# Performance work log

Measured on AMD Instinct MI355X. Metric: run time of the kernel, lower is better.

## Reference

```python
import jax, jax.numpy as jnp
import numpy as np
from jax.scipy.special import erf

B, T, D, H = 256, 128, 128, 1024  # batch, seq_len, enc_in, hid_dim
SIGMA = 0.5  # stochastic-gate sigma (STG FeatureSelector)


def _uniform(key, shape, std):
    return jax.random.uniform(key, shape, jnp.float32, -std, std)


def setup_inputs() -> dict:
    key = jax.random.key(0)
    ks = jax.random.split(key, 16)
    std = 1.0 / np.sqrt(H)
    inp = {
        "x": jax.random.normal(ks[0], (B, T, D), jnp.float32),
        # s_lstm
        "s_x2h_w": _uniform(ks[1], (4 * H, D), std),
        "s_x2h_b": _uniform(ks[2], (4 * H,), std),
        "s_h2h_w": _uniform(ks[3], (4 * H, H), std),
        "s_h2h_b": _uniform(ks[4], (4 * H,), std),
        # p_lstm
        "p_x2h_w": _uniform(ks[5], (4 * H, D), std),
        "p_x2h_b": _uniform(ks[6], (4 * H,), std),
        "p_h2h_w": _uniform(ks[7], (4 * H, H), std),
        "p_h2h_b": _uniform(ks[8], (4 * H,), std),
        # p_fc: hid -> 2*enc_in
        "p_fc_w": _uniform(ks[9], (2 * D, H), std),
        "p_fc_b": _uniform(ks[10], (2 * D,), std),
        # FeatureSelector mu layer: hid -> enc_in
        "fs_w": _uniform(ks[11], (D, H), std),
        "fs_b": _uniform(ks[12], (D,), std),
    }
    return inp


def _lstm_cell(x, h, c, wx, bx, wh, bh):
    gates = x @ wx.T + bx + h @ wh.T + bh          # [B, 4H]
    i, f, g, o = jnp.split(gates, 4, axis=1)
    cy = c * jax.nn.sigmoid(f) + jax.nn.sigmoid(i) * jnp.tanh(g)
    hy = jax.nn.sigmoid(o) * jnp.tanh(cy)
    return hy, cy


def _forward(x, s_x2h_w, s_x2h_b, s_h2h_w, s_h2h_b,
             p_x2h_w, p_x2h_b, p_h2h_w, p_h2h_b,
             p_fc_w, p_fc_b, fs_w, fs_b):
    b = x.shape[0]
    xt = jnp.swapaxes(x, 0, 1)  # [T, B, D] time-major
    sqrt2 = jnp.sqrt(jnp.float32(2.0))

    def step(carry, xs):
        hn, cn, hn2, cn2, mask_prev, xhat0_prev = carry
        x_t, x_tp1 = xs
        # at seq==0 mask_prev=1, xhat0_prev=0 -> input is exactly x_t
        inp = mask_prev * x_t + (1.0 - mask_prev) * xhat0_prev
        hn, cn = _lstm_cell(inp, hn, cn, s_x2h_w, s_x2h_b, s_h2h_w, s_h2h_b)
        # FeatureSelector (eval: noise = 0)
        mu = hn @ fs_w.T + fs_b                     # [B, D]
        z = mu
        mask = jnp.clip(z + 0.5, 0.0, 1.0)          # hard sigmoid gate
        reg = 0.5 * (1.0 + erf((mu + 0.5) / (SIGMA * sqrt2)))  # Phi((mu+0.5)/sigma)
        hn2, cn2 = _lstm_cell(mask * x_tp1, hn2, cn2, p_x2h_w, p_x2h_b, p_h2h_w, p_h2h_b)
        xhat = (hn2 @ p_fc_w.T + p_fc_b).reshape(b, 2, D)
        xhat0, xhat1 = xhat[:, 0, :], xhat[:, 1, :]
        mu_det = jax.lax.stop_gradient(mu)          # torch.tensor(numpy) detaches
        prob_det = jax.lax.stop_gradient(reg)
        outs = (mask, xhat0, xhat1, reg, mu_det, prob_det, z)
        return (hn, cn, hn2, cn2, mask, xhat0), outs

    h0 = jnp.zeros((b, H), x.dtype)
    carry0 = (h0, h0, h0, h0, jnp.ones((b, D), x.dtype), jnp.zeros((b, D), x.dtype))
    _, outs = jax.lax.scan(step, carry0, (xt[:-1], xt[1:]))
    # each out: [T-1, B, D] -> [B, T-1, D]
    return tuple(jnp.swapaxes(o, 0, 1) for o in outs)


def reference(x, s_x2h_w, s_x2h_b, s_h2h_w, s_h2h_b,
              p_x2h_w, p_x2h_b, p_h2h_w, p_h2h_b,
              p_fc_w, p_fc_b, fs_w, fs_b):
    return _forward(x, s_x2h_w, s_x2h_b, s_h2h_w, s_h2h_b,
                    p_x2h_w, p_x2h_b, p_h2h_w, p_h2h_b,
                    p_fc_w, p_fc_b, fs_w, fs_b)
```

## Files before the change

### kernel.cpp

```cpp
#include <hip/hip_runtime.h>
#include <math.h>

#define BB 256
#define TT 128
#define DD 128
#define HH 1024
#define G4 4096
#define TOUT 127
#define OSZ (BB * TOUT * DD)
#define NKB 36
#define ACTE (16 * NKB * 512)

typedef __bf16 bf16x8 __attribute__((ext_vector_type(8)));
typedef float f32x4 __attribute__((ext_vector_type(4)));
typedef unsigned short u16;
typedef unsigned int u32;
typedef unsigned long long u64;

#define MFMA16 __builtin_amdgcn_mfma_f32_16x16x32_bf16

__device__ inline u16 f2bf(float f) {
    union { float f; u32 u; } v; v.f = f;
    u32 r = v.u + 0x7FFFu + ((v.u >> 16) & 1u);
    return (u16)(r >> 16);
}
__device__ inline float fsig(float x)  { return __fdividef(1.0f, 1.0f + __expf(-x)); }
__device__ inline float ftanh(float x) { return __fdividef(2.0f, 1.0f + __expf(-2.0f * x)) - 1.0f; }

__device__ __forceinline__ bf16x8 ld_act(const u16* p) {
    union { u64 q[2]; bf16x8 v; } u;
    u.q[0] = __hip_atomic_load((u64*)p,     __ATOMIC_RELAXED, __HIP_MEMORY_SCOPE_AGENT);
    u.q[1] = __hip_atomic_load((u64*)p + 1, __ATOMIC_RELAXED, __HIP_MEMORY_SCOPE_AGENT);
    return u.v;
}
__device__ __forceinline__ void st_u32(u16* p, u32 v) {
    __hip_atomic_store((u32*)p, v, __ATOMIC_RELAXED, __HIP_MEMORY_SCOPE_AGENT);
}

__device__ __forceinline__ void gbar(u32* bars, u32 gen) {
    asm volatile("s_waitcnt vmcnt(0)" ::: "memory");
    __syncthreads();
    if (threadIdx.x == 0)
        __hip_atomic_fetch_add(&bars[(blockIdx.x & 31) << 4], 1u,
                               __ATOMIC_RELAXED, __HIP_MEMORY_SCOPE_AGENT);
    if (threadIdx.x < 32) {
        while (__hip_atomic_load(&bars[threadIdx.x << 4],
                                 __ATOMIC_RELAXED, __HIP_MEMORY_SCOPE_AGENT) < gen * 8u)
            __builtin_amdgcn_s_sleep(4);
    }
    __syncthreads();
}

struct SArgs {
    u16 *acts, *actp;
    const u16 *wS, *wP, *fswb, *pfcb;
    const float *bS, *bP, *fsb, *pfb, *x;
    float* mbuf;
    float* out;
    u32* bars;
};

__device__ __forceinline__ void lstm_phase(
    const u16* __restrict__ act, const u16* __restrict__ wb,
    const float* __restrict__ bias, float* __restrict__ cst ,
    u16* __restrict__ hact, float* __restrict__ red ,
    u64* __restrict__ a_lds ,
    int bid, int w, int lane)
{
    const int tid = threadIdx.x;
    const int bm = bid >> 5, bn = bid & 31;
    const int kg = w >> 2, wv = w & 3;

    {
        const u64* src = (const u64*)(act + (size_t)bm * 2 * NKB * 512);
#pragma unroll
        for (int u = 0; u < 18; ++u) {
            int idx = tid + u * 512;
            a_lds[idx] = __hip_atomic_load(&src[idx], __ATOMIC_RELAXED,
                                           __HIP_MEMORY_SCOPE_AGENT);
        }
    }
    __syncthreads();

    const u16* ab = (const u16*)a_lds;
    const u16* a0p = ab + (((0 * NKB) + kg * 18) * 64 + lane) * 8;
    const u16* a1p = ab + (((1 * NKB) + kg * 18) * 64 + lane) * 8;
    const u16* b0p = wb + (((size_t)(bn * 8 + wv * 2 + 0) * NKB + kg * 18) * 64 + lane) * 8;
    const u16* b1p = wb + (((size_t)(bn * 8 + wv * 2 + 1) * NKB + kg * 18) * 64 + lane) * 8;

    f32x4 acc[2][2] = {};
    bf16x8 bc0 = *(const bf16x8*)(b0p);
    bf16x8 bc1 = *(const bf16x8*)(b1p);
#pragma unroll 6
    for (int it = 0; it < 18; ++it) {
        bf16x8 bn0, bn1;
        if (it < 17) {
            bn0 = *(const bf16x8*)(b0p + (it + 1) * 512);
            bn1 = *(const bf16x8*)(b1p + (it + 1) * 512);
        }
        bf16x8 a0 = *(const bf16x8*)(a0p + it * 512);
        bf16x8 a1 = *(const bf16x8*)(a1p + it * 512);
        acc[0][0] = MFMA16(a0, bc0, acc[0][0], 0, 0, 0);
        acc[0][1] = MFMA16(a0, bc1, acc[0][1], 0, 0, 0);
        acc[1][0] = MFMA16(a1, bc0, acc[1][0], 0, 0, 0);
        acc[1][1] = MFMA16(a1, bc1, acc[1][1], 0, 0, 0);
        if (it < 17) { bc0 = bn0; bc1 = bn1; }
    }

    if (kg == 1) {
#pragma unroll
        for (int mi = 0; mi < 2; ++mi)
#pragma unroll
        for (int bi = 0; bi < 2; ++bi)
            *(f32x4*)&red[(((((wv << 1) | mi) << 1) | bi) << 8) + (lane << 2)] = acc[mi][bi];
    }
    __syncthreads();

    if (kg == 0) {
        const int col = lane & 15, row4 = (lane >> 4) << 2, g0 = lane & 3;
#pragma unroll
        for (int mi = 0; mi < 2; ++mi)
#pragma unroll
        for (int bi = 0; bi < 2; ++bi) {
            f32x4 s1 = *(const f32x4*)&red[(((((wv << 1) | mi) << 1) | bi) << 8) + (lane << 2)];
            const int n = bn * 128 + (wv * 2 + bi) * 16 + col;
            const float bv = bias[n];
#pragma unroll
            for (int rr = 0; rr < 4; ++rr) {
                float v = acc[mi][bi][rr] + s1[rr] + bv;
                float v1 = __shfl_xor(v, 1);
                float v2 = __shfl_xor(v, 2);
                float v3 = __shfl_xor(v, 3);
                const int m = bm * 32 + mi * 16 + row4 + rr;
                const int j = n >> 2;
                u32 hbits = 0;
                if (g0 == 0) {
                    const int ml = mi * 16 + row4 + rr;
                    const int jl = j - bn * 32;
                    float cp = cst[ml * 32 + jl];
                    float cy = cp * fsig(v1) + fsig(v) * ftanh(v2);
                    float hy = fsig(v3) * ftanh(cy);
                    cst[ml * 32 + jl] = cy;
                    hbits = (u32)f2bf(hy);
                }
                u32 pv = hbits | (((u32)__shfl_xor((int)hbits, 4)) << 16);
                if ((lane & 7) == 0)
                    st_u32(&hact[(((size_t)(m >> 4) * NKB + (4 + (j >> 5))) * 64 +
                                  ((m & 15) + (((j >> 3) & 3) << 4))) * 8 + (j & 7)], pv);
            }
        }
    }
}

__global__ __launch_bounds__(512, 2) void k_scan(SArgs A)
{
    __shared__ __align__(16) u64 a_lds[9216];
    __shared__ __align__(16) float red[4096];
    __shared__ float cst[2][32][32];

    const int bid = blockIdx.x, tid = threadIdx.x;
    const int w = tid >> 6, lane = tid & 63;

    for (int i = tid; i < 2 * 32 * 32; i += 512) ((float*)cst)[i] = 0.f;

    float* o_mask = A.out;
    float* o_x0   = A.out + 1 * (size_t)OSZ;
    float* o_x1   = A.out + 2 * (size_t)OSZ;
    float* o_reg  = A.out + 3 * (size_t)OSZ;
    float* o_mu   = A.out + 4 * (size_t)OSZ;
    float* o_prob = A.out + 5 * (size_t)OSZ;
    float* o_z    = A.out + 6 * (size_t)OSZ;

    u32 gen = 0;

    for (int t = 0; t < TOUT; ++t) {
        const u16* s_cur = A.acts + (size_t)(t & 1) * ACTE;
        u16*       s_nxt = A.acts + (size_t)((t + 1) & 1) * ACTE;
        u16*       p_cur = A.actp + (size_t)(t & 1) * ACTE;
        u16*       p_nxt = A.actp + (size_t)((t + 1) & 1) * ACTE;

        lstm_phase(s_cur, A.wS, A.bS, &cst[0][0][0], s_nxt, red, a_lds, bid, w, lane);
        gbar(A.bars, ++gen);

        if (bid < 128) {
            const int bm = bid >> 3, bn = bid & 7;
            f32x4 acc = {};
#pragma unroll
            for (int i = 0; i < 4; ++i) {
                const int kb = (w << 2) + i;
                bf16x8 av = ld_act(s_nxt + (((size_t)bm * NKB + 4 + kb) * 64 + lane) * 8);
                bf16x8 bv = *(const bf16x8*)(A.fswb + (((size_t)bn * 32 + kb) * 64 + lane) * 8);
                acc = MFMA16(av, bv, acc, 0, 0, 0);
            }
            *(f32x4*)&red[(w * 64 + lane) << 2] = acc;
            __syncthreads();
            if (tid < 256) {
                const int m16 = tid >> 4, d16 = tid & 15;
                const int rl = ((m16 >> 2) << 4) | d16, rr = m16 & 3;
                float v = 0.f;
#pragma unroll
                for (int ww = 0; ww < 8; ++ww) v += red[((ww * 64 + rl) << 2) + rr];
                const int m = (bm << 4) + m16, d = (bn << 4) + d16;
                float mu = v + A.fsb[d];
                float mask = fminf(fmaxf(mu + 0.5f, 0.f), 1.f);
                float reg = 0.5f * (1.0f + erff((mu + 0.5f) * 1.41421356237f));
                const size_t o = (size_t)m * (TOUT * DD) + (size_t)t * DD + d;
                o_mask[o] = mask; o_reg[o] = reg; o_mu[o] = mu; o_prob[o] = reg; o_z[o] = mu;
                __hip_atomic_store(&A.mbuf[m * DD + d], mask,
                                   __ATOMIC_RELAXED, __HIP_MEMORY_SCOPE_AGENT);
                float xv = A.x[(size_t)m * (TT * DD) + (size_t)(t + 1) * DD + d];
                u32 xb = (u32)f2bf(mask * xv);
                u32 pv = xb | (((u32)__shfl_xor((int)xb, 1)) << 16);
                if ((d16 & 1) == 0)
                    st_u32(&p_cur[(((size_t)(m >> 4) * NKB + (d >> 5)) * 64 +
                                   ((m & 15) + (((d >> 3) & 3) << 4))) * 8 + (d & 7)], pv);
            }
        }
        gbar(A.bars, ++gen);

        lstm_phase(p_cur, A.wP, A.bP, &cst[1][0][0], p_nxt, red, a_lds, bid, w, lane);
        gbar(A.bars, ++gen);

        {
            const int bm = bid >> 4, bn = bid & 15;
            f32x4 acc = {};
#pragma unroll
            for (int i = 0; i < 4; ++i) {
                const int kb = (w << 2) + i;
                bf16x8 av = ld_act(p_nxt + (((size_t)bm * NKB + 4 + kb) * 64 + lane) * 8);
                bf16x8 bv = *(const bf16x8*)(A.pfcb + (((size_t)bn * 32 + kb) * 64 + lane) * 8);
                acc = MFMA16(av, bv, acc, 0, 0, 0);
            }
            *(f32x4*)&red[(w * 64 + lane) << 2] = acc;
            __syncthreads();
            if (tid < 256) {
                const int m16 = tid >> 4, d16 = tid & 15;
                const int rl = ((m16 >> 2) << 4) | d16, rr = m16 & 3;
                float v = 0.f;
#pragma unroll
                for (int ww = 0; ww < 8; ++ww) v += red[((ww * 64 + rl) << 2) + rr];
                const int m = (bm << 4) + m16, n = (bn << 4) + d16;
                v += A.pfb[n];
                const size_t ob = (size_t)m * (TOUT * DD) + (size_t)t * DD;
                if (bn < 8) {
                    o_x0[ob + n] = v;
                    float mk = __hip_atomic_load(&A.mbuf[m * DD + n],
                                                 __ATOMIC_RELAXED, __HIP_MEMORY_SCOPE_AGENT);
                    float xv = A.x[(size_t)m * (TT * DD) + (size_t)(t + 1) * DD + n];
                    u32 ib = (u32)f2bf(mk * xv + (1.f - mk) * v);
                    u32 pv = ib | (((u32)__shfl_xor((int)ib, 1)) << 16);
                    if ((d16 & 1) == 0)
                        st_u32(&s_nxt[(((size_t)(m >> 4) * NKB + (n >> 5)) * 64 +
                                       ((m & 15) + (((n >> 3) & 3) << 4))) * 8 + (n & 7)], pv);
                } else {
                    o_x1[ob + (n - DD)] = v;
                }
            }
        }
        gbar(A.bars, ++gen);
    }
}


__global__ void k_wgates(const float* __restrict__ wx, const float* __restrict__ wh,
                         u16* __restrict__ blob) {
    int i = blockIdx.x * 256 + threadIdx.x;
    if (i >= 256 * NKB * 64) return;
    int lane = i & 63, cblk = (i >> 6) % NKB, rblk = (i >> 6) / NKB;
    int n = (rblk << 4) | (lane & 15);
    int c = (cblk << 5) + ((lane >> 4) << 3);
    int orow = ((n & 3) << 10) | (n >> 2);
    const float* s = (cblk < 4) ? (wx + (size_t)orow * DD + c)
                                : (wh + (size_t)orow * HH + (c - 128));
    u16* d = blob + (size_t)i * 8;
#pragma unroll
    for (int k = 0; k < 8; ++k) d[k] = f2bf(s[k]);
}

__global__ void k_wplain(const float* __restrict__ wsrc, u16* __restrict__ blob,
                         int nblk, int K) {
    int CB = K >> 5;
    int i = blockIdx.x * 256 + threadIdx.x;
    if (i >= nblk * CB * 64) return;
    int lane = i & 63, cblk = (i >> 6) % CB, rblk = (i >> 6) / CB;
    int r = (rblk << 4) | (lane & 15);
    int c = (cblk << 5) + ((lane >> 4) << 3);
    const float* s = wsrc + (size_t)r * K + c;
    u16* d = blob + (size_t)i * 8;
#pragma unroll
    for (int k = 0; k < 8; ++k) d[k] = f2bf(s[k]);
}

__global__ void k_bias2(const float* __restrict__ bx, const float* __restrict__ bh,
                        float* __restrict__ dst) {
    int r = blockIdx.x * 256 + threadIdx.x;
    if (r < G4) {
        int o = ((r & 3) << 10) | (r >> 2);
        dst[r] = bx[o] + bh[o];
    }
}

__global__ void k_zero(u16* acts, u16* actp, u32* bars) {
    size_t i = (size_t)blockIdx.x * 256 + threadIdx.x;
    if (i < 2 * (size_t)ACTE) { acts[i] = 0; actp[i] = 0; }
    if (i < 512) bars[i] = 0;
}

__global__ void k_fillx(const float* __restrict__ x, u16* __restrict__ acts) {
    int i = blockIdx.x * 256 + threadIdx.x;
    if (i >= BB * DD) return;
    int m = i >> 7, d = i & 127;
    acts[(((size_t)(m >> 4) * NKB + (d >> 5)) * 64 +
          ((m & 15) + (((d >> 3) & 3) << 4))) * 8 + (d & 7)] =
        f2bf(x[(size_t)m * (TT * DD) + d]);
}

extern "C" void kernel_launch(void* const* d_in, const int* in_sizes, int n_in,
                              void* d_out, int out_size, void* d_ws, size_t ws_size,
                              hipStream_t stream) {
    const float* x       = (const float*)d_in[0];
    const float* s_x2h_w = (const float*)d_in[1];
    const float* s_x2h_b = (const float*)d_in[2];
    const float* s_h2h_w = (const float*)d_in[3];
    const float* s_h2h_b = (const float*)d_in[4];
    const float* p_x2h_w = (const float*)d_in[5];
    const float* p_x2h_b = (const float*)d_in[6];
    const float* p_h2h_w = (const float*)d_in[7];
    const float* p_h2h_b = (const float*)d_in[8];
    const float* p_fc_w  = (const float*)d_in[9];
    const float* p_fc_b  = (const float*)d_in[10];
    const float* fs_w    = (const float*)d_in[11];
    const float* fs_b    = (const float*)d_in[12];

    char* ws = (char*)d_ws;
    size_t off = 0;
    auto alloc = [&](size_t bytes) { void* p = ws + off; off += (bytes + 255) & ~(size_t)255; return p; };
    u16*   wS   = (u16*)  alloc((size_t)G4 * 1152 * 2);
    u16*   wP   = (u16*)  alloc((size_t)G4 * 1152 * 2);
    u16*   fswb = (u16*)  alloc((size_t)8 * 32 * 512 * 2);
    u16*   pfcb = (u16*)  alloc((size_t)16 * 32 * 512 * 2);
    float* bS   = (float*)alloc((size_t)G4 * 4);
    float* bP   = (float*)alloc((size_t)G4 * 4);
    u16*   acts = (u16*)  alloc((size_t)2 * ACTE * 2);
    u16*   actp = (u16*)  alloc((size_t)2 * ACTE * 2);
    float* mbuf = (float*)alloc((size_t)BB * DD * 4);
    u32*   bars = (u32*)  alloc(2048);

    k_wgates<<<dim3(2304), 256, 0, stream>>>(s_x2h_w, s_h2h_w, wS);
    k_wgates<<<dim3(2304), 256, 0, stream>>>(p_x2h_w, p_h2h_w, wP);
    k_wplain<<<dim3(64),  256, 0, stream>>>(fs_w, fswb, 8, 1024);
    k_wplain<<<dim3(128), 256, 0, stream>>>(p_fc_w, pfcb, 16, 1024);
    k_bias2<<<dim3(16), 256, 0, stream>>>(s_x2h_b, s_h2h_b, bS);
    k_bias2<<<dim3(16), 256, 0, stream>>>(p_x2h_b, p_h2h_b, bP);
    k_zero<<<dim3(2304), 256, 0, stream>>>(acts, actp, bars);
    k_fillx<<<dim3(128), 256, 0, stream>>>(x, acts);

    SArgs sa;
    sa.acts = acts; sa.actp = actp;
    sa.wS = wS; sa.wP = wP; sa.fswb = fswb; sa.pfcb = pfcb;
    sa.bS = bS; sa.bP = bP; sa.fsb = fs_b; sa.pfb = p_fc_b; sa.x = x;
    sa.mbuf = mbuf; sa.out = (float*)d_out; sa.bars = bars;

    void* kargs[] = { &sa };
    hipError_t e = hipLaunchCooperativeKernel((const void*)k_scan, dim3(256), dim3(512),
                                              kargs, 0, stream);
    if (e != hipSuccess) {
        k_scan<<<dim3(256), dim3(512), 0, stream>>>(sa);
    }
}
```

Baseline: 5.063 ms.

## Overlap FS/FC heads with next LSTM h2h GEMM using flag-based sync

Restructures the persistent scan so the recurrent h2h part of each LSTM gate GEMM (K=1024, from an LDS copy prefetched during the previous phase) overlaps with the feature-selector and p_fc GEMMs, done by a subset of waves. Point-to-point per-tile flags replace two of the four grid barriers per step, and the x-input slice (K=128) is added afterward in a tail. The grid barrier is centralized: block 0 polls the counters and publishes an epoch. The K-split reduction through shared memory is removed, with each wave doing the full K for one column tile. This cuts barrier count and serialization per timestep, at the cost of more complex synchronization and one block per CU.

```diff
diff --git a/kernel.cpp b/kernel.cpp
--- a/kernel.cpp
+++ b/kernel.cpp
@@ -27,237 +27,290 @@
 __device__ inline float fsig(float x)  { return __fdividef(1.0f, 1.0f + __expf(-x)); }
 __device__ inline float ftanh(float x) { return __fdividef(2.0f, 1.0f + __expf(-2.0f * x)) - 1.0f; }
 
-__device__ __forceinline__ bf16x8 ld_act(const u16* p) {
+__device__ __forceinline__ u64 ldc64(const u64* p) {
+    return __hip_atomic_load(p, __ATOMIC_RELAXED, __HIP_MEMORY_SCOPE_AGENT);
+}
+__device__ __forceinline__ bf16x8 ldc128(const u16* p) {
     union { u64 q[2]; bf16x8 v; } u;
-    u.q[0] = __hip_atomic_load((u64*)p,     __ATOMIC_RELAXED, __HIP_MEMORY_SCOPE_AGENT);
-    u.q[1] = __hip_atomic_load((u64*)p + 1, __ATOMIC_RELAXED, __HIP_MEMORY_SCOPE_AGENT);
+    u.q[0] = ldc64((const u64*)p);
+    u.q[1] = ldc64((const u64*)p + 1);
     return u.v;
 }
-__device__ __forceinline__ void st_u32(u16* p, u32 v) {
+__device__ __forceinline__ void stc32(u16* p, u32 v) {
     __hip_atomic_store((u32*)p, v, __ATOMIC_RELAXED, __HIP_MEMORY_SCOPE_AGENT);
 }
-
-__device__ __forceinline__ void gbar(u32* bars, u32 gen) {
+__device__ __forceinline__ void stcf(float* p, float v) {
+    __hip_atomic_store(p, v, __ATOMIC_RELAXED, __HIP_MEMORY_SCOPE_AGENT);
+}
+__device__ __forceinline__ float ldcf(const float* p) {
+    return __hip_atomic_load(p, __ATOMIC_RELAXED, __HIP_MEMORY_SCOPE_AGENT);
+}
+
+struct SArgs {
+    u16 *acts, *actp;
+    const u16 *wS, *wP, *fswb, *pfcb;
+    const float *bS, *bP, *fsb, *pfb, *x;
+    float *mbuf, *out;
+    u32 *bars, *epoch, *flags;
+};
+
+__device__ __forceinline__ void gbar(u32* bars, u32* epoch, u32 gen) {
     asm volatile("s_waitcnt vmcnt(0)" ::: "memory");
     __syncthreads();
     if (threadIdx.x == 0)
         __hip_atomic_fetch_add(&bars[(blockIdx.x & 31) << 4], 1u,
                                __ATOMIC_RELAXED, __HIP_MEMORY_SCOPE_AGENT);
-    if (threadIdx.x < 32) {
+    if (blockIdx.x == 0 && threadIdx.x < 32) {
         while (__hip_atomic_load(&bars[threadIdx.x << 4],
                                  __ATOMIC_RELAXED, __HIP_MEMORY_SCOPE_AGENT) < gen * 8u)
-            __builtin_amdgcn_s_sleep(4);
+            __builtin_amdgcn_s_sleep(1);
+        if (threadIdx.x == 0)
+            __hip_atomic_store(epoch, gen, __ATOMIC_RELAXED, __HIP_MEMORY_SCOPE_AGENT);
+    }
+    if (threadIdx.x == 0) {
+        while (__hip_atomic_load(epoch, __ATOMIC_RELAXED, __HIP_MEMORY_SCOPE_AGENT) < gen)
+            __builtin_amdgcn_s_sleep(1);
     }
     __syncthreads();
 }
 
-struct SArgs {
-    u16 *acts, *actp;
-    const u16 *wS, *wP, *fswb, *pfcb;
-    const float *bS, *bP, *fsb, *pfb, *x;
-    float* mbuf;
-    float* out;
-    u32* bars;
-};
-
-__device__ __forceinline__ void lstm_phase(
-    const u16* __restrict__ act, const u16* __restrict__ wb,
-    const float* __restrict__ bias, float* __restrict__ cst ,
-    u16* __restrict__ hact, float* __restrict__ red ,
-    u64* __restrict__ a_lds ,
-    int bid, int w, int lane)
+__device__ __forceinline__ void gates_tail(
+    const SArgs& A, f32x4 acc0, f32x4 acc1,
+    const u16* xpart, const u16* wb, const float* bias,
+    float* cm, u16* hout, int bm, int bn, int w, int lane)
 {
-    const int tid = threadIdx.x;
+#pragma unroll
+    for (int kb = 0; kb < 4; ++kb) {
+        bf16x8 a0 = ldc128(xpart + (size_t)kb * 512 + lane * 8);
+        bf16x8 a1 = ldc128(xpart + (size_t)(36 + kb) * 512 + lane * 8);
+        bf16x8 bv = *(const bf16x8*)(wb + ((size_t)(bn * 8 + w) * 36 + kb) * 512 + lane * 8);
+        acc0 = MFMA16(a0, bv, acc0, 0, 0, 0);
+        acc1 = MFMA16(a1, bv, acc1, 0, 0, 0);
+    }
+    const int col = lane & 15, row4 = (lane >> 4) << 2, g0 = lane & 3;
+    const int n = bn * 128 + w * 16 + col;
+    const int j = n >> 2;
+    const float bvv = bias[n];
+    const int jl = w * 4 + (col >> 2);
+#pragma unroll
+    for (int mi = 0; mi < 2; ++mi) {
+        f32x4 av = mi ? acc1 : acc0;
+#pragma unroll
+        for (int rr = 0; rr < 4; ++rr) {
+            float v = av[rr] + bvv;
+            float v1 = __shfl_xor(v, 1), v2 = __shfl_xor(v, 2), v3 = __shfl_xor(v, 3);
+            const int m = bm * 32 + mi * 16 + row4 + rr;
+            u32 hb = 0;
+            if (g0 == 0) {
+                const int ml = mi * 16 + row4 + rr;
+                float cp = cm[ml * 32 + jl];
+                float cy = cp * fsig(v1) + fsig(v) * ftanh(v2);
+                float hy = fsig(v3) * ftanh(cy);
+                cm[ml * 32 + jl] = cy;
+                hb = (u32)f2bf(hy);
+            }
+            u32 pv = hb | (((u32)__shfl_xor((int)hb, 4)) << 16);
+            if ((lane & 7) == 0)
+                stc32(&hout[((size_t)(m >> 4) * 36 + (4 + (j >> 5))) * 512 +
+                            ((m & 15) + (((j >> 3) & 3) << 4)) * 8 + (j & 7)], pv);
+        }
+    }
+}
+
+template<int TASK>
+__device__ __forceinline__ void gphase(
+    const SArgs& A, int t, int bid, int tid, int w, int lane,
+    const u64* a_rd, u64* a_wr, const u64* pre_src,
+    const u16* xpart, const u16* wb, const float* bias,
+    float* cm, u16* hout)
+{
     const int bm = bid >> 5, bn = bid & 31;
-    const int kg = w >> 2, wv = w & 3;
-
-    {
-        const u64* src = (const u64*)(act + (size_t)bm * 2 * NKB * 512);
-#pragma unroll
-        for (int u = 0; u < 18; ++u) {
-            int idx = tid + u * 512;
-            a_lds[idx] = __hip_atomic_load(&src[idx], __ATOMIC_RELAXED,
-                                           __HIP_MEMORY_SCOPE_AGENT);
-        }
-    }
-    __syncthreads();
-
-    const u16* ab = (const u16*)a_lds;
-    const u16* a0p = ab + (((0 * NKB) + kg * 18) * 64 + lane) * 8;
-    const u16* a1p = ab + (((1 * NKB) + kg * 18) * 64 + lane) * 8;
-    const u16* b0p = wb + (((size_t)(bn * 8 + wv * 2 + 0) * NKB + kg * 18) * 64 + lane) * 8;
-    const u16* b1p = wb + (((size_t)(bn * 8 + wv * 2 + 1) * NKB + kg * 18) * 64 + lane) * 8;
-
-    f32x4 acc[2][2] = {};
-    bf16x8 bc0 = *(const bf16x8*)(b0p);
-    bf16x8 bc1 = *(const bf16x8*)(b1p);
-#pragma unroll 6
-    for (int it = 0; it < 18; ++it) {
-        bf16x8 bn0, bn1;
-        if (it < 17) {
-            bn0 = *(const bf16x8*)(b0p + (it + 1) * 512);
-            bn1 = *(const bf16x8*)(b1p + (it + 1) * 512);
-        }
-        bf16x8 a0 = *(const bf16x8*)(a0p + it * 512);
-        bf16x8 a1 = *(const bf16x8*)(a1p + it * 512);
-        acc[0][0] = MFMA16(a0, bc0, acc[0][0], 0, 0, 0);
-        acc[0][1] = MFMA16(a0, bc1, acc[0][1], 0, 0, 0);
-        acc[1][0] = MFMA16(a1, bc0, acc[1][0], 0, 0, 0);
-        acc[1][1] = MFMA16(a1, bc1, acc[1][1], 0, 0, 0);
-        if (it < 17) { bc0 = bn0; bc1 = bn1; }
-    }
-
-    if (kg == 1) {
-#pragma unroll
-        for (int mi = 0; mi < 2; ++mi)
-#pragma unroll
-        for (int bi = 0; bi < 2; ++bi)
-            *(f32x4*)&red[(((((wv << 1) | mi) << 1) | bi) << 8) + (lane << 2)] = acc[mi][bi];
-    }
-    __syncthreads();
-
-    if (kg == 0) {
-        const int col = lane & 15, row4 = (lane >> 4) << 2, g0 = lane & 3;
-#pragma unroll
-        for (int mi = 0; mi < 2; ++mi)
-#pragma unroll
-        for (int bi = 0; bi < 2; ++bi) {
-            f32x4 s1 = *(const f32x4*)&red[(((((wv << 1) | mi) << 1) | bi) << 8) + (lane << 2)];
-            const int n = bn * 128 + (wv * 2 + bi) * 16 + col;
-            const float bv = bias[n];
+    const bool dotask = (TASK == 1) ? (bid < 16) : (bid < 32);
+    const int tau = bid * 8 + w;
+
+    const u16 *tA = nullptr, *tB = nullptr;
+    if (dotask) {
+        if (TASK == 1) {
+            const int mg = tau >> 3, dg = tau & 7;
+            tA = A.acts + ((size_t)mg * 36 + 4) * 512 + lane * 8;
+            tB = A.fswb + (size_t)(dg * 32) * 512 + lane * 8;
+        } else {
+            const int mg = tau >> 4, ng = tau & 15;
+            tA = A.actp + ((size_t)mg * 36 + 4) * 512 + lane * 8;
+            tB = A.pfcb + (size_t)(ng * 32) * 512 + lane * 8;
+        }
+    }
+
+    f32x4 acc0 = {}, acc1 = {}, tacc = {};
+    const bf16x8* Ard = (const bf16x8*)a_rd;
+    const u16* bp = wb + ((size_t)(bn * 8 + w) * 36 + 4) * 512 + lane * 8;
+    bf16x8 bcur = *(const bf16x8*)bp;
+
+#pragma unroll 1
+    for (int g = 0; g < 4; ++g) {
+        u64 pr0, pr1, pr2, pr3;
+        {
+            const int pb = g * 2048 + tid;
+            int p;
+            p = pb;        pr0 = ldc64(pre_src + ((p >> 12) * 4608 + 512 + (p & 4095)));
+            p = pb + 512;  pr1 = ldc64(pre_src + ((p >> 12) * 4608 + 512 + (p & 4095)));
+            p = pb + 1024; pr2 = ldc64(pre_src + ((p >> 12) * 4608 + 512 + (p & 4095)));
+            p = pb + 1536; pr3 = ldc64(pre_src + ((p >> 12) * 4608 + 512 + (p & 4095)));
+        }
+#pragma unroll
+        for (int i = 0; i < 8; ++i) {
+            const int it = g * 8 + i;
+            bf16x8 bnx = *(const bf16x8*)(bp + (size_t)((it < 31) ? (it + 1) : it) * 512);
+            bf16x8 a0 = Ard[(size_t)it * 64 + lane];
+            bf16x8 a1 = Ard[(size_t)(32 + it) * 64 + lane];
+            acc0 = MFMA16(a0, bcur, acc0, 0, 0, 0);
+            acc1 = MFMA16(a1, bcur, acc1, 0, 0, 0);
+            if (dotask) {
+                bf16x8 tav = ldc128(tA + (size_t)it * 512);
+                bf16x8 tbv = *(const bf16x8*)(tB + (size_t)it * 512);
+                tacc = MFMA16(tav, tbv, tacc, 0, 0, 0);
+            }
+            bcur = bnx;
+        }
+        {
+            const int pb = g * 2048 + tid;
+            a_wr[pb] = pr0; a_wr[pb + 512] = pr1;
+            a_wr[pb + 1024] = pr2; a_wr[pb + 1536] = pr3;
+        }
+    }
+
+    if (dotask) {
+        const int col = lane & 15, row4 = (lane >> 4) << 2;
+        if (TASK == 1) {
+            const int mg = tau >> 3, dg = tau & 7;
+            const int d = dg * 16 + col;
+            const float bv = A.fsb[d];
 #pragma unroll
             for (int rr = 0; rr < 4; ++rr) {
-                float v = acc[mi][bi][rr] + s1[rr] + bv;
-                float v1 = __shfl_xor(v, 1);
-                float v2 = __shfl_xor(v, 2);
-                float v3 = __shfl_xor(v, 3);
-                const int m = bm * 32 + mi * 16 + row4 + rr;
-                const int j = n >> 2;
-                u32 hbits = 0;
-                if (g0 == 0) {
-                    const int ml = mi * 16 + row4 + rr;
-                    const int jl = j - bn * 32;
-                    float cp = cst[ml * 32 + jl];
-                    float cy = cp * fsig(v1) + fsig(v) * ftanh(v2);
-                    float hy = fsig(v3) * ftanh(cy);
-                    cst[ml * 32 + jl] = cy;
-                    hbits = (u32)f2bf(hy);
-                }
-                u32 pv = hbits | (((u32)__shfl_xor((int)hbits, 4)) << 16);
-                if ((lane & 7) == 0)
-                    st_u32(&hact[(((size_t)(m >> 4) * NKB + (4 + (j >> 5))) * 64 +
-                                  ((m & 15) + (((j >> 3) & 3) << 4))) * 8 + (j & 7)], pv);
-            }
-        }
-    }
-}
-
-__global__ __launch_bounds__(512, 2) void k_scan(SArgs A)
-{
-    __shared__ __align__(16) u64 a_lds[9216];
-    __shared__ __align__(16) float red[4096];
-    __shared__ float cst[2][32][32];
-
-    const int bid = blockIdx.x, tid = threadIdx.x;
-    const int w = tid >> 6, lane = tid & 63;
-
-    for (int i = tid; i < 2 * 32 * 32; i += 512) ((float*)cst)[i] = 0.f;
-
-    float* o_mask = A.out;
-    float* o_x0   = A.out + 1 * (size_t)OSZ;
-    float* o_x1   = A.out + 2 * (size_t)OSZ;
-    float* o_reg  = A.out + 3 * (size_t)OSZ;
-    float* o_mu   = A.out + 4 * (size_t)OSZ;
-    float* o_prob = A.out + 5 * (size_t)OSZ;
-    float* o_z    = A.out + 6 * (size_t)OSZ;
-
-    u32 gen = 0;
-
-    for (int t = 0; t < TOUT; ++t) {
-        const u16* s_cur = A.acts + (size_t)(t & 1) * ACTE;
-        u16*       s_nxt = A.acts + (size_t)((t + 1) & 1) * ACTE;
-        u16*       p_cur = A.actp + (size_t)(t & 1) * ACTE;
-        u16*       p_nxt = A.actp + (size_t)((t + 1) & 1) * ACTE;
-
-        lstm_phase(s_cur, A.wS, A.bS, &cst[0][0][0], s_nxt, red, a_lds, bid, w, lane);
-        gbar(A.bars, ++gen);
-
-        if (bid < 128) {
-            const int bm = bid >> 3, bn = bid & 7;
-            f32x4 acc = {};
-#pragma unroll
-            for (int i = 0; i < 4; ++i) {
-                const int kb = (w << 2) + i;
-                bf16x8 av = ld_act(s_nxt + (((size_t)bm * NKB + 4 + kb) * 64 + lane) * 8);
-                bf16x8 bv = *(const bf16x8*)(A.fswb + (((size_t)bn * 32 + kb) * 64 + lane) * 8);
-                acc = MFMA16(av, bv, acc, 0, 0, 0);
-            }
-            *(f32x4*)&red[(w * 64 + lane) << 2] = acc;
-            __syncthreads();
-            if (tid < 256) {
-                const int m16 = tid >> 4, d16 = tid & 15;
-                const int rl = ((m16 >> 2) << 4) | d16, rr = m16 & 3;
-                float v = 0.f;
-#pragma unroll
-                for (int ww = 0; ww < 8; ++ww) v += red[((ww * 64 + rl) << 2) + rr];
-                const int m = (bm << 4) + m16, d = (bn << 4) + d16;
-                float mu = v + A.fsb[d];
+                const int m = mg * 16 + row4 + rr;
+                float mu = tacc[rr] + bv;
                 float mask = fminf(fmaxf(mu + 0.5f, 0.f), 1.f);
-                float reg = 0.5f * (1.0f + erff((mu + 0.5f) * 1.41421356237f));
+                float reg = 0.5f * (1.f + erff((mu + 0.5f) * 1.41421356237f));
                 const size_t o = (size_t)m * (TOUT * DD) + (size_t)t * DD + d;
-                o_mask[o] = mask; o_reg[o] = reg; o_mu[o] = mu; o_prob[o] = reg; o_z[o] = mu;
-                __hip_atomic_store(&A.mbuf[m * DD + d], mask,
-                                   __ATOMIC_RELAXED, __HIP_MEMORY_SCOPE_AGENT);
+                A.out[o] = mask;
+                A.out[o + 3 * (size_t)OSZ] = reg;
+                A.out[o + 4 * (size_t)OSZ] = mu;
+                A.out[o + 5 * (size_t)OSZ] = reg;
+                A.out[o + 6 * (size_t)OSZ] = mu;
+                stcf(&A.mbuf[m * DD + d], mask);
                 float xv = A.x[(size_t)m * (TT * DD) + (size_t)(t + 1) * DD + d];
                 u32 xb = (u32)f2bf(mask * xv);
                 u32 pv = xb | (((u32)__shfl_xor((int)xb, 1)) << 16);
-                if ((d16 & 1) == 0)
-                    st_u32(&p_cur[(((size_t)(m >> 4) * NKB + (d >> 5)) * 64 +
-                                   ((m & 15) + (((d >> 3) & 3) << 4))) * 8 + (d & 7)], pv);
+                if ((lane & 1) == 0)
+                    stc32(&A.actp[((size_t)(m >> 4) * 36 + (d >> 5)) * 512 +
+                                  ((m & 15) + (((d >> 3) & 3) << 4)) * 8 + (d & 7)], pv);
             }
-        }
-        gbar(A.bars, ++gen);
-
-        lstm_phase(p_cur, A.wP, A.bP, &cst[1][0][0], p_nxt, red, a_lds, bid, w, lane);
-        gbar(A.bars, ++gen);
-
-        {
-            const int bm = bid >> 4, bn = bid & 15;
-            f32x4 acc = {};
-#pragma unroll
-            for (int i = 0; i < 4; ++i) {
-                const int kb = (w << 2) + i;
-                bf16x8 av = ld_act(p_nxt + (((size_t)bm * NKB + 4 + kb) * 64 + lane) * 8);
-                bf16x8 bv = *(const bf16x8*)(A.pfcb + (((size_t)bn * 32 + kb) * 64 + lane) * 8);
-                acc = MFMA16(av, bv, acc, 0, 0, 0);
-            }
-            *(f32x4*)&red[(w * 64 + lane) << 2] = acc;
-            __syncthreads();
-            if (tid < 256) {
-                const int m16 = tid >> 4, d16 = tid & 15;
-                const int rl = ((m16 >> 2) << 4) | d16, rr = m16 & 3;
-                float v = 0.f;
-#pragma unroll
-                for (int ww = 0; ww < 8; ++ww) v += red[((ww * 64 + rl) << 2) + rr];
-                const int m = (bm << 4) + m16, n = (bn << 4) + d16;
-                v += A.pfb[n];
+        } else {
+            const int mg = tau >> 4, ng = tau & 15;
+            const int n = ng * 16 + col;
+            const float bv = A.pfb[n];
+#pragma unroll
+            for (int rr = 0; rr < 4; ++rr) {
+                const int m = mg * 16 + row4 + rr;
+                float v = tacc[rr] + bv;
                 const size_t ob = (size_t)m * (TOUT * DD) + (size_t)t * DD;
-                if (bn < 8) {
-                    o_x0[ob + n] = v;
-                    float mk = __hip_atomic_load(&A.mbuf[m * DD + n],
-                                                 __ATOMIC_RELAXED, __HIP_MEMORY_SCOPE_AGENT);
+                if (ng < 8) {
+                    A.out[ob + n + (size_t)OSZ] = v;
+                    float mk = ldcf(&A.mbuf[m * DD + n]);
                     float xv = A.x[(size_t)m * (TT * DD) + (size_t)(t + 1) * DD + n];
                     u32 ib = (u32)f2bf(mk * xv + (1.f - mk) * v);
                     u32 pv = ib | (((u32)__shfl_xor((int)ib, 1)) << 16);
-                    if ((d16 & 1) == 0)
-                        st_u32(&s_nxt[(((size_t)(m >> 4) * NKB + (n >> 5)) * 64 +
-                                       ((m & 15) + (((n >> 3) & 3) << 4))) * 8 + (n & 7)], pv);
+                    if ((lane & 1) == 0)
+                        stc32(&A.acts[((size_t)(m >> 4) * 36 + (n >> 5)) * 512 +
+                                      ((m & 15) + (((n >> 3) & 3) << 4)) * 8 + (n & 7)], pv);
                 } else {
-                    o_x1[ob + (n - DD)] = v;
+                    A.out[ob + (n - DD) + 2 * (size_t)OSZ] = v;
                 }
             }
         }
-        gbar(A.bars, ++gen);
+        asm volatile("s_waitcnt vmcnt(0)" ::: "memory");
+        if (lane == 0) {
+            const int f = (TASK == 1) ? tau : (128 + tau);
+            __hip_atomic_store(&A.flags[f << 4], (u32)(t + 1),
+                               __ATOMIC_RELAXED, __HIP_MEMORY_SCOPE_AGENT);
+        }
+    }
+
+    if (w == 0 && lane < 16) {
+        const int f = (TASK == 1) ? (16 * bm + lane)
+                                  : (128 + 32 * bm + (lane & 7) + ((lane >> 3) << 4));
+        const u32 need = (u32)(t + 1);
+        while (__hip_atomic_load(&A.flags[f << 4],
+                                 __ATOMIC_RELAXED, __HIP_MEMORY_SCOPE_AGENT) < need)
+            __builtin_amdgcn_s_sleep(1);
+    }
+    __syncthreads();
+
+    gates_tail(A, acc0, acc1, xpart, wb, bias, cm, hout, bm, bn, w, lane);
+}
+
+__global__ __launch_bounds__(512, 1) void k_scan(SArgs A)
+{
+    __shared__ __align__(16) u64 aS[8192];
+    __shared__ __align__(16) u64 aP[8192];
+    __shared__ float cst[2][32][32];
+
+    const int bid = blockIdx.x, tid = threadIdx.x;
+    const int w = tid >> 6, lane = tid & 63;
+    const int bm = bid >> 5;
+
+    for (int i = tid; i < 2 * 32 * 32; i += 512) ((float*)cst)[i] = 0.f;
+    for (int i = tid; i < 8192; i += 512) aP[i] = 0;
+    __syncthreads();
+
+    u32 gen = 0;
+
+    {
+        f32x4 z0 = {}, z1 = {};
+        gates_tail(A, z0, z1, A.acts + (size_t)(2 * bm) * 36 * 512, A.wS, A.bS,
+                   &cst[0][0][0], A.acts, bm, bid & 31, w, lane);
+        gbar(A.bars, A.epoch, ++gen);
+    }
+
+    for (int t = 0; t < TOUT; ++t) {
+        gphase<1>(A, t, bid, tid, w, lane, aP, aS,
+                  (const u64*)A.acts + (size_t)(2 * bm) * 4608,
+                  A.actp + (size_t)(2 * bm) * 36 * 512,
+                  A.wP, A.bP, &cst[1][0][0], A.actp);
+        gbar(A.bars, A.epoch, ++gen);
+
+        if (t < TOUT - 1) {
+            gphase<2>(A, t, bid, tid, w, lane, aS, aP,
+                      (const u64*)A.actp + (size_t)(2 * bm) * 4608,
+                      A.acts + (size_t)(2 * bm) * 36 * 512,
+                      A.wS, A.bS, &cst[0][0][0], A.acts);
+            gbar(A.bars, A.epoch, ++gen);
+        } else {
+            if (bid < 32) {
+                const int tau = bid * 8 + w;
+                const int mg = tau >> 4, ng = tau & 15;
+                const u16* tA = A.actp + ((size_t)mg * 36 + 4) * 512 + lane * 8;
+                const u16* tB = A.pfcb + (size_t)(ng * 32) * 512 + lane * 8;
+                f32x4 tacc = {};
+#pragma unroll 8
+                for (int it = 0; it < 32; ++it) {
+                    bf16x8 tav = ldc128(tA + (size_t)it * 512);
+                    bf16x8 tbv = *(const bf16x8*)(tB + (size_t)it * 512);
+                    tacc = MFMA16(tav, tbv, tacc, 0, 0, 0);
+                }
+                const int col = lane & 15, row4 = (lane >> 4) << 2;
+                const int n = ng * 16 + col;
+                const float bv = A.pfb[n];
+#pragma unroll
+                for (int rr = 0; rr < 4; ++rr) {
+                    const int m = mg * 16 + row4 + rr;
+                    float v = tacc[rr] + bv;
+                    const size_t ob = (size_t)m * (TOUT * DD) + (size_t)t * DD;
+                    if (ng < 8) A.out[ob + n + (size_t)OSZ] = v;
+                    else        A.out[ob + (n - DD) + 2 * (size_t)OSZ] = v;
+                }
+            }
+        }
     }
 }
 
@@ -300,10 +353,14 @@
     }
 }
 
-__global__ void k_zero(u16* acts, u16* actp, u32* bars) {
+__global__ void k_zero(u16* acts, u16* actp, float* mbuf,
+                       u32* bars, u32* epoch, u32* flags) {
     size_t i = (size_t)blockIdx.x * 256 + threadIdx.x;
-    if (i < 2 * (size_t)ACTE) { acts[i] = 0; actp[i] = 0; }
+    if (i < (size_t)ACTE) { acts[i] = 0; actp[i] = 0; }
+    if (i < (size_t)BB * DD) mbuf[i] = 0.f;
     if (i < 512) bars[i] = 0;
+    if (i < 16) epoch[i] = 0;
+    if (i < 6144) flags[i] = 0;
 }
 
 __global__ void k_fillx(const float* __restrict__ x, u16* __restrict__ acts) {
@@ -335,16 +392,18 @@
     char* ws = (char*)d_ws;
     size_t off = 0;
     auto alloc = [&](size_t bytes) { void* p = ws + off; off += (bytes + 255) & ~(size_t)255; return p; };
-    u16*   wS   = (u16*)  alloc((size_t)G4 * 1152 * 2);
-    u16*   wP   = (u16*)  alloc((size_t)G4 * 1152 * 2);
-    u16*   fswb = (u16*)  alloc((size_t)8 * 32 * 512 * 2);
-    u16*   pfcb = (u16*)  alloc((size_t)16 * 32 * 512 * 2);
-    float* bS   = (float*)alloc((size_t)G4 * 4);
-    float* bP   = (float*)alloc((size_t)G4 * 4);
-    u16*   acts = (u16*)  alloc((size_t)2 * ACTE * 2);
-    u16*   actp = (u16*)  alloc((size_t)2 * ACTE * 2);
-    float* mbuf = (float*)alloc((size_t)BB * DD * 4);
-    u32*   bars = (u32*)  alloc(2048);
+    u16*   wS    = (u16*)  alloc((size_t)G4 * 1152 * 2);
+    u16*   wP    = (u16*)  alloc((size_t)G4 * 1152 * 2);
+    u16*   fswb  = (u16*)  alloc((size_t)8 * 32 * 512 * 2);
+    u16*   pfcb  = (u16*)  alloc((size_t)16 * 32 * 512 * 2);
+    float* bS    = (float*)alloc((size_t)G4 * 4);
+    float* bP    = (float*)alloc((size_t)G4 * 4);
+    u16*   acts  = (u16*)  alloc((size_t)ACTE * 2);
+    u16*   actp  = (u16*)  alloc((size_t)ACTE * 2);
+    float* mbuf  = (float*)alloc((size_t)BB * DD * 4);
+    u32*   bars  = (u32*)  alloc(512 * 4);
+    u32*   epoch = (u32*)  alloc(16 * 4);
+    u32*   flags = (u32*)  alloc(6144 * 4);
 
     k_wgates<<<dim3(2304), 256, 0, stream>>>(s_x2h_w, s_h2h_w, wS);
     k_wgates<<<dim3(2304), 256, 0, stream>>>(p_x2h_w, p_h2h_w, wP);
@@ -352,14 +411,15 @@
     k_wplain<<<dim3(128), 256, 0, stream>>>(p_fc_w, pfcb, 16, 1024);
     k_bias2<<<dim3(16), 256, 0, stream>>>(s_x2h_b, s_h2h_b, bS);
     k_bias2<<<dim3(16), 256, 0, stream>>>(p_x2h_b, p_h2h_b, bP);
-    k_zero<<<dim3(2304), 256, 0, stream>>>(acts, actp, bars);
+    k_zero<<<dim3(1152), 256, 0, stream>>>(acts, actp, mbuf, bars, epoch, flags);
     k_fillx<<<dim3(128), 256, 0, stream>>>(x, acts);
 
     SArgs sa;
     sa.acts = acts; sa.actp = actp;
     sa.wS = wS; sa.wP = wP; sa.fswb = fswb; sa.pfcb = pfcb;
     sa.bS = bS; sa.bP = bP; sa.fsb = fs_b; sa.pfb = p_fc_b; sa.x = x;
-    sa.mbuf = mbuf; sa.out = (float*)d_out; sa.bars = bars;
+    sa.mbuf = mbuf; sa.out = (float*)d_out;
+    sa.bars = bars; sa.epoch = epoch; sa.flags = flags;
 
     void* kargs[] = { &sa };
     hipError_t e = hipLaunchCooperativeKernel((const void*)k_scan, dim3(256), dim3(512),
```

Measured after the change: 5.509 ms, median of 5. +8.8%, slower.
